# Performance work log

Measured on AMD Instinct MI355X. Metric: run time of the kernel, lower is better.

Reference implementation:

```python
import jax, jax.numpy as jnp
import numpy as np

LMAX = 3
KMAX = [128, 96, 64, 32]   # k_max_l, decreasing in l
N_ATOMS = 10000
N_EDGES = 100000
N_RADIAL = 8
CUTOFF = 5.0

def _bounds(l):
    lo = KMAX[l + 1] if l < LMAX else 0
    return lo, KMAX[l]

def _uncouple(split_list, U):
    # split_list: per l' in 0..L, [n, 2l'+1, k]; U: [3**L, (L+1)**2]
    x = jnp.concatenate(split_list, axis=1)      # [n, (L+1)**2, k]
    return jnp.einsum('dm,nmk->ndk', U, x)       # [n, 3**L, k]

def _couple(f, U, L):
    x = jnp.einsum('dm,ndk->nmk', U, f)          # [n, (L+1)**2, k]
    out, off = [], 0
    for lp in range(L + 1):
        out.append(x[:, off:off + 2 * lp + 1, :])
        off += 2 * lp + 1
    return out

def _forward(r, sh, feat, Wrad, U, Wlin, centers, neighbors):
    # radial basis with smooth cutoff, then per-l channel embedding
    n = jnp.arange(1, N_RADIAL + 1, dtype=r.dtype)
    rb = jnp.sin(n * jnp.pi * r[:, None] / CUTOFF) / (r[:, None] + 1e-6)
    fc = 0.5 * (jnp.cos(jnp.pi * jnp.clip(r / CUTOFF, 0.0, 1.0)) + 1.0)
    rb = rb * fc[:, None]                        # [E, N_RADIAL]
    radial = [rb @ Wrad[l] for l in range(LMAX + 1)]          # [E, KMAX[l]]
    vexp = [sh[l] * radial[l][:, None, :] for l in range(LMAX + 1)]  # [E, 2l+1, KMAX[l]]

    def group(ts, l):
        lo, hi = _bounds(l)
        return [ts[lp][:, :, lo:hi] for lp in range(l + 1)]

    unc_v = [_uncouple(group(vexp, l), U[l]) for l in range(LMAX + 1)]
    unc_f = [_uncouple(group(feat, l), U[l]) for l in range(LMAX + 1)]
    # neighbor gather + elementwise combine in the uncoupled (Cartesian) space
    combined = [unc_v[l] * unc_f[l][neighbors] for l in range(LMAX + 1)]
    # scatter-add pooling over centers (index_add_ equivalent)
    pooled = [jax.ops.segment_sum(c, centers, num_segments=N_ATOMS) for c in combined]
    coupled = [_couple(pooled[l], U[l], l) for l in range(LMAX + 1)]
    cat = [jnp.concatenate([coupled[lp][l] for lp in range(l, LMAX + 1)], axis=-1)
           for l in range(LMAX + 1)]             # [n_atoms, 2l+1, KMAX[l]]
    # NOTE: mp_scaling multiply in the original is dead code (result unused)
    out = [feat[l] + jnp.einsum('nmk,kq->nmq', cat[l], Wlin[l]) for l in range(LMAX + 1)]
    return tuple(out)

def setup_inputs() -> dict:
    key = jax.random.key(0)
    ks = jax.random.split(key, 40)
    inp = {'r': jax.random.uniform(ks[0], (N_EDGES,), minval=0.5, maxval=CUTOFF, dtype=jnp.float32)}
    for l in range(LMAX + 1):
        k = KMAX[l]
        inp[f'sh{l}'] = jax.random.normal(ks[1 + l], (N_EDGES, 2 * l + 1, 1), dtype=jnp.float32)
        inp[f'feat{l}'] = jax.random.normal(ks[5 + l], (N_ATOMS, 2 * l + 1, k), dtype=jnp.float32)
        inp[f'Wrad{l}'] = jax.random.normal(ks[9 + l], (N_RADIAL, k), dtype=jnp.float32) / np.sqrt(N_RADIAL).astype(np.float32)
        inp[f'U{l}'] = jax.random.normal(ks[13 + l], (3 ** l, (l + 1) ** 2), dtype=jnp.float32) / np.float32(np.sqrt((l + 1) ** 2))
        inp[f'Wlin{l}'] = jax.random.normal(ks[17 + l], (k, k), dtype=jnp.float32) / np.sqrt(k).astype(np.float32)
    inp['centers'] = jax.random.randint(ks[21], (N_EDGES,), 0, N_ATOMS, dtype=jnp.int32)
    inp['neighbors'] = jax.random.randint(ks[22], (N_EDGES,), 0, N_ATOMS, dtype=jnp.int32)
    return inp

def reference(r, sh0, sh1, sh2, sh3, feat0, feat1, feat2, feat3,
              Wrad0, Wrad1, Wrad2, Wrad3, U0, U1, U2, U3,
              Wlin0, Wlin1, Wlin2, Wlin3, centers, neighbors):
    return _forward(r, [sh0, sh1, sh2, sh3], [feat0, feat1, feat2, feat3],
                    [Wrad0, Wrad1, Wrad2, Wrad3], [U0, U1, U2, U3],
                    [Wlin0, Wlin1, Wlin2, Wlin3], centers, neighbors)
```

## Files before the change

### kernel.cpp

```cpp
#include <hip/hip_runtime.h>
#include <hip/hip_fp16.h>
#include <math.h>

#define NA 10000
#define NE 100000
#define PI_F 3.14159265358979323846f


__device__ __forceinline__ constexpr int rowC(int row) {
    return (row == 0) ? 0 : (row < 4) ? 1 : (row < 13) ? 2 : 3;
}

__device__ __forceinline__ void stage_U(const float* __restrict__ U0,
                                        const float* __restrict__ U1,
                                        const float* __restrict__ U2,
                                        const float* __restrict__ U3,
                                        float* uLds, int t, int nthr) {
    for (int i = t; i < 526; i += nthr) {
        float v;
        if (i == 0)       v = U0[0];
        else if (i < 13)  v = U1[i - 1];
        else if (i < 94)  v = U2[i - 13];
        else              v = U3[i - 94];
        uLds[i] = v;
    }
}

__global__ __launch_bounds__(256) void kCount(const int* __restrict__ centers,
                                              int* __restrict__ counts)
{
    const int e = blockIdx.x * 256 + threadIdx.x;
    if (e < NE) atomicAdd(&counts[centers[e]], 1);
}

__global__ __launch_bounds__(1024) void kScan(const int* __restrict__ counts,
                                              int* __restrict__ offsets,
                                              int* __restrict__ cursor)
{
    __shared__ int sums[1024];
    const int t = threadIdx.x;
    const int base = t * 10;
    int local[10];
    int s = 0;
#pragma unroll
    for (int j = 0; j < 10; ++j) {
        int idx = base + j;
        int v = (idx < NA) ? counts[idx] : 0;
        local[j] = s;
        s += v;
    }
    sums[t] = s;
    __syncthreads();
    for (int off = 1; off < 1024; off <<= 1) {
        int v = (t >= off) ? sums[t - off] : 0;
        __syncthreads();
        sums[t] += v;
        __syncthreads();
    }
    const int prev = (t == 0) ? 0 : sums[t - 1];
#pragma unroll
    for (int j = 0; j < 10; ++j) {
        int idx = base + j;
        if (idx <= NA) {
            int o = prev + local[j];
            offsets[idx] = o;
            if (idx < NA) cursor[idx] = o;
        }
    }
}

__global__ __launch_bounds__(256) void kPrep(
    const float* __restrict__ f0, const float* __restrict__ f1,
    const float* __restrict__ f2, const float* __restrict__ f3,
    const float* __restrict__ r,
    const float* __restrict__ sh0, const float* __restrict__ sh1,
    const float* __restrict__ sh2, const float* __restrict__ sh3,
    const float* __restrict__ U0, const float* __restrict__ U1,
    const float* __restrict__ U2, const float* __restrict__ U3,
    const int* __restrict__ centers, const int* __restrict__ neighbors,
    int* __restrict__ cursor,
    uint4* __restrict__ uncf16, float* __restrict__ rbbuf,
    uint2* __restrict__ csh, int* __restrict__ nbrs)
{
    __shared__ float uLds[526];
    const int t = threadIdx.x;
    stage_U(U0, U1, U2, U3, uLds, t, 256);
    __syncthreads();

    if (blockIdx.x < 1250) {
        const int la = t >> 5, k = t & 31;
        const int a = blockIdx.x * 8 + la;
        float arr[40];

        {
            arr[0] = uLds[0] * f0[(size_t)a * 128 + 96 + k];
        }
        {
            float x[4];
            x[0] = f0[(size_t)a * 128 + 64 + k];
#pragma unroll
            for (int m = 0; m < 3; ++m) x[1 + m] = f1[(size_t)a * 288 + m * 96 + 64 + k];
#pragma unroll
            for (int d = 0; d < 3; ++d) {
                float acc = 0.f;
#pragma unroll
                for (int m = 0; m < 4; ++m) acc += uLds[1 + d * 4 + m] * x[m];
                arr[1 + d] = acc;
            }
        }
        {
            float x[9];
            x[0] = f0[(size_t)a * 128 + 32 + k];
#pragma unroll
            for (int m = 0; m < 3; ++m) x[1 + m] = f1[(size_t)a * 288 + m * 96 + 32 + k];
#pragma unroll
            for (int m = 0; m < 5; ++m) x[4 + m] = f2[(size_t)a * 320 + m * 64 + 32 + k];
#pragma unroll
            for (int d = 0; d < 9; ++d) {
                float acc = 0.f;
#pragma unroll
                for (int m = 0; m < 9; ++m) acc += uLds[13 + d * 9 + m] * x[m];
                arr[4 + d] = acc;
            }
        }
        {
            float x[16];
            x[0] = f0[(size_t)a * 128 + k];
#pragma unroll
            for (int m = 0; m < 3; ++m) x[1 + m] = f1[(size_t)a * 288 + m * 96 + k];
#pragma unroll
            for (int m = 0; m < 5; ++m) x[4 + m] = f2[(size_t)a * 320 + m * 64 + k];
#pragma unroll
            for (int m = 0; m < 7; ++m) x[9 + m] = f3[(size_t)a * 224 + m * 32 + k];
#pragma unroll
            for (int d = 0; d < 27; ++d) {
                float acc = 0.f;
#pragma unroll
                for (int m = 0; m < 16; ++m) acc += uLds[94 + d * 16 + m] * x[m];
                arr[13 + d] = acc;
            }
        }
        uint4* op = uncf16 + (size_t)a * 160 + k;
#pragma unroll
        for (int jj = 0; jj < 5; ++jj) {
            uint4 w;
            __half2 h0 = __floats2half2_rn(arr[8 * jj + 0], arr[8 * jj + 1]);
            __half2 h1 = __floats2half2_rn(arr[8 * jj + 2], arr[8 * jj + 3]);
            __half2 h2 = __floats2half2_rn(arr[8 * jj + 4], arr[8 * jj + 5]);
            __half2 h3 = __floats2half2_rn(arr[8 * jj + 6], arr[8 * jj + 7]);
            w.x = *(unsigned int*)&h0; w.y = *(unsigned int*)&h1;
            w.z = *(unsigned int*)&h2; w.w = *(unsigned int*)&h3;
            op[jj * 32] = w;
        }
    } else {
        const int e = (blockIdx.x - 1250) * 256 + t;
        if (e >= NE) return;

        const int c_ = centers[e];
        const int pos = atomicAdd(&cursor[c_], 1);
        nbrs[pos] = neighbors[e];

        float shv[16];
        shv[0] = sh0[e];
#pragma unroll
        for (int m = 0; m < 3; ++m) shv[1 + m] = sh1[(size_t)e * 3 + m];
#pragma unroll
        for (int m = 0; m < 5; ++m) shv[4 + m] = sh2[(size_t)e * 5 + m];
#pragma unroll
        for (int m = 0; m < 7; ++m) shv[9 + m] = sh3[(size_t)e * 7 + m];

        const float rv = r[e];
        const float fc = 0.5f * (cosf(PI_F * fminf(rv * 0.2f, 1.0f)) + 1.0f);
        const float pref = fc / (rv + 1e-6f);
        const float step = rv * (PI_F * 0.2f);
        float4 ra, rb;
        ra.x = sinf(1.f * step) * pref; ra.y = sinf(2.f * step) * pref;
        ra.z = sinf(3.f * step) * pref; ra.w = sinf(4.f * step) * pref;
        rb.x = sinf(5.f * step) * pref; rb.y = sinf(6.f * step) * pref;
        rb.z = sinf(7.f * step) * pref; rb.w = sinf(8.f * step) * pref;
        *(float4*)(rbbuf + (size_t)pos * 8)     = ra;
        *(float4*)(rbbuf + (size_t)pos * 8 + 4) = rb;

        const int UO[4] = {0, 1, 13, 94};
        const int RO[4] = {0, 1, 4, 13};
        const int P3[4] = {1, 3, 9, 27};
        uint2* cso = csh + (size_t)pos * 40;
#pragma unroll
        for (int c = 0; c < 4; ++c) {
            const int M2 = (c + 1) * (c + 1);
            for (int d = 0; d < P3[c]; ++d) {
                float cv[4] = {0.f, 0.f, 0.f, 0.f};
#pragma unroll
                for (int lp = 0; lp < 4; ++lp) {
                    if (lp > c) break;
                    float s = 0.f;
#pragma unroll
                    for (int ml = 0; ml < 2 * lp + 1; ++ml)
                        s += uLds[UO[c] + d * M2 + lp * lp + ml] * shv[lp * lp + ml];
                    cv[lp] = s;
                }
                __half2 h0 = __floats2half2_rn(cv[0], cv[1]);
                __half2 h1 = __floats2half2_rn(cv[2], cv[3]);
                uint2 u;
                u.x = *(unsigned int*)&h0;
                u.y = *(unsigned int*)&h1;
                cso[RO[c] + d] = u;
            }
        }
    }
}

__global__ __launch_bounds__(256, 2) void kB2(
    const float* __restrict__ Wr0, const float* __restrict__ Wr1,
    const float* __restrict__ Wr2, const float* __restrict__ Wr3,
    const int* __restrict__ offsets, const int* __restrict__ nbrs,
    const float* __restrict__ rbbuf, const uint2* __restrict__ csh,
    const uint4* __restrict__ uncf16, float* __restrict__ pooled)
{
    __shared__ float wLds[2560];
    const int t = threadIdx.x;
    for (int i = t; i < 2560; i += 256) {
        float v;
        if (i < 1024)      v = Wr0[i];
        else if (i < 1792) v = Wr1[i - 1024];
        else if (i < 2304) v = Wr2[i - 1792];
        else               v = Wr3[i - 2304];
        wLds[i] = v;
    }
    __syncthreads();

    const int lane = t & 63;
    const int wv = t >> 6;
    const int k = lane & 31;
    const int g2 = lane >> 5;
    const int a = blockIdx.x * 4 + wv;
    const int beg = offsets[a], end = offsets[a + 1];

    float acc[40];
#pragma unroll
    for (int i = 0; i < 40; ++i) acc[i] = 0.f;

    const int KL[4] = {128, 96, 64, 32};
    const int WO[4] = {0, 1024, 1792, 2304};

    int i = beg + g2;
    int nbr = (i < end) ? nbrs[i] : 0;
    for (; i < end; i += 2) {
        const int nbr_nx = (i + 2 < end) ? nbrs[i + 2] : 0;

        const uint4* up = uncf16 + (size_t)nbr * 160 + k;
        const uint4 w0 = up[0 * 32];
        const uint4 w1 = up[1 * 32];
        const uint4 w2 = up[2 * 32];
        const uint4 w3 = up[3 * 32];
        const uint4 w4 = up[4 * 32];

        const float4 r0 = *(const float4*)(rbbuf + (size_t)i * 8);
        const float4 r1 = *(const float4*)(rbbuf + (size_t)i * 8 + 4);
        const float rb[8] = {r0.x, r0.y, r0.z, r0.w, r1.x, r1.y, r1.z, r1.w};

        float rad[4][4];
#pragma unroll
        for (int lp = 0; lp < 4; ++lp) {
#pragma unroll
            for (int c = 0; c < 4; ++c) {
                if (c < lp) continue;
                const int base = 32 * (3 - c);
                float s = 0.f;
#pragma unroll
                for (int n = 0; n < 8; ++n)
                    s += rb[n] * wLds[WO[lp] + n * KL[lp] + base + k];
                rad[lp][c] = s;
            }
        }

        const uint2* cs = csh + (size_t)i * 40;
        const uint4 ww[5] = {w0, w1, w2, w3, w4};
#pragma unroll
        for (int jj = 0; jj < 5; ++jj) {
            const unsigned int ws[4] = {ww[jj].x, ww[jj].y, ww[jj].z, ww[jj].w};
#pragma unroll
            for (int p2 = 0; p2 < 4; ++p2) {
                const int row0 = 8 * jj + 2 * p2, row1 = row0 + 1;
                const int c0 = rowC(row0), c1 = rowC(row1);
                const __half2 h = *(const __half2*)&ws[p2];
                const uint2 ua = cs[row0];
                const uint2 ub = cs[row1];
                const __half2 a01 = *(const __half2*)&ua.x;
                const __half2 a23 = *(const __half2*)&ua.y;
                const __half2 b01 = *(const __half2*)&ub.x;
                const __half2 b23 = *(const __half2*)&ub.y;
                float uv0 = __low2float(a01) * rad[0][c0];
                if (c0 >= 1) uv0 += __high2float(a01) * rad[1][c0];
                if (c0 >= 2) uv0 += __low2float(a23) * rad[2][c0];
                if (c0 >= 3) uv0 += __high2float(a23) * rad[3][c0];
                float uv1 = __low2float(b01) * rad[0][c1];
                if (c1 >= 1) uv1 += __high2float(b01) * rad[1][c1];
                if (c1 >= 2) uv1 += __low2float(b23) * rad[2][c1];
                if (c1 >= 3) uv1 += __high2float(b23) * rad[3][c1];
                acc[row0] += uv0 * __low2float(h);
                acc[row1] += uv1 * __high2float(h);
            }
        }
        nbr = nbr_nx;
    }

#pragma unroll
    for (int row = 0; row < 40; ++row) acc[row] += __shfl_xor(acc[row], 32);

    float* pp = pooled + (size_t)a * 1280 + k;
#pragma unroll
    for (int rr = 0; rr < 20; ++rr) {
        const float v   = g2 ? acc[rr + 20] : acc[rr];
        const int  row  = g2 ? (rr + 20)    : rr;
        pp[row * 32] = v;
    }
}

__global__ __launch_bounds__(256) void kC_out(
    const float* __restrict__ pooled,
    const float* __restrict__ f0, const float* __restrict__ f1,
    const float* __restrict__ f2, const float* __restrict__ f3,
    const float* __restrict__ U0, const float* __restrict__ U1,
    const float* __restrict__ U2, const float* __restrict__ U3,
    const float* __restrict__ W0, const float* __restrict__ W1,
    const float* __restrict__ W2, const float* __restrict__ W3,
    float* __restrict__ out)
{
    __shared__ float uLds[526];
    __shared__ float plds[4 * 1280];
    __shared__ float clds[120 * 33];
    const int t = threadIdx.x;
    stage_U(U0, U1, U2, U3, uLds, t, 256);
    const int a0 = blockIdx.x * 4;
    {
        const float4* src = (const float4*)(pooled + (size_t)a0 * 1280);
        float4* dst = (float4*)plds;
        for (int i = t; i < 1280; i += 256) dst[i] = src[i];
    }
    __syncthreads();

    if (t < 128) {
        const int la = t >> 5, kk = t & 31;
        clds[(la * 30 + 0) * 33 + kk] = uLds[0] * plds[la * 1280 + 0 * 32 + kk];
    }
#pragma unroll
    for (int s = t; s < 512; s += 256) {
        const int la = s >> 7, rem = s & 127;
        const int m = rem >> 5, kk = rem & 31;
        float acc = 0.f;
#pragma unroll
        for (int d = 0; d < 3; ++d)
            acc += uLds[1 + d * 4 + m] * plds[la * 1280 + (1 + d) * 32 + kk];
        clds[(la * 30 + 1 + m) * 33 + kk] = acc;
    }
    for (int s = t; s < 1152; s += 256) {
        const int la = s / 288, rem = s - la * 288;
        const int m = rem >> 5, kk = rem & 31;
        float acc = 0.f;
#pragma unroll
        for (int d = 0; d < 9; ++d)
            acc += uLds[13 + d * 9 + m] * plds[la * 1280 + (4 + d) * 32 + kk];
        clds[(la * 30 + 5 + m) * 33 + kk] = acc;
    }
    for (int s = t; s < 2048; s += 256) {
        const int la = s >> 9, rem = s & 511;
        const int m = rem >> 5, kk = rem & 31;
        float acc = 0.f;
#pragma unroll
        for (int d = 0; d < 27; ++d)
            acc += uLds[94 + d * 16 + m] * plds[la * 1280 + (13 + d) * 32 + kk];
        clds[(la * 30 + 14 + m) * 33 + kk] = acc;
    }
    __syncthreads();

    int l, m, q;
    bool active = true;
    if (t < 32)       { l = 0; m = 0;                               q = 4 * t; }
    else if (t < 104) { l = 1; int u = t - 32;  m = u / 24; q = 4 * (u % 24); }
    else if (t < 184) { l = 2; int u = t - 104; m = u / 16; q = 4 * (u % 16); }
    else if (t < 240) { l = 3; int u = t - 184; m = u / 8;  q = 4 * (u % 8);  }
    else active = false;

    if (active) {
        const int K  = (l == 0) ? 128 : (l == 1) ? 96 : (l == 2) ? 64 : 32;
        const int MK = (l == 0) ? 128 : (l == 1) ? 288 : (l == 2) ? 320 : 224;
        const size_t Ol = (l == 0) ? 0 : (l == 1) ? 1280000 : (l == 2) ? 4160000 : 7360000;
        const float* F = (l == 0) ? f0 : (l == 1) ? f1 : (l == 2) ? f2 : f3;
        const float* W = (l == 0) ? W0 : (l == 1) ? W1 : (l == 2) ? W2 : W3;
        const int CRB[4] = {0, 1, 5, 14};

        float4 acc[4];
#pragma unroll
        for (int la = 0; la < 4; ++la)
            acc[la] = *(const float4*)(F + (size_t)(a0 + la) * MK + m * K + q);

        for (int j = 0; j < 4 - l; ++j) {
            const int c = l + j;
            const int crow = CRB[c] + l * l + m;
#pragma unroll
            for (int kk = 0; kk < 32; ++kk) {
                const float4 w = *(const float4*)(W + (size_t)(32 * j + kk) * K + q);
#pragma unroll
                for (int la = 0; la < 4; ++la) {
                    const float cv = clds[(la * 30 + crow) * 33 + kk];
                    acc[la].x += cv * w.x; acc[la].y += cv * w.y;
                    acc[la].z += cv * w.z; acc[la].w += cv * w.w;
                }
            }
        }
#pragma unroll
        for (int la = 0; la < 4; ++la)
            *(float4*)(out + Ol + (size_t)(a0 + la) * MK + m * K + q) = acc[la];
    }
}

extern "C" void kernel_launch(void* const* d_in, const int* in_sizes, int n_in,
                              void* d_out, int out_size, void* d_ws, size_t ws_size,
                              hipStream_t stream)
{
    int ir, ish[4], ift[4], iwr[4], iu[4], iwl[4], ic, in_;
    if (in_sizes[2] == 300000) {
        ir = 0;
        for (int l = 0; l < 4; ++l) { ish[l] = 1 + l; ift[l] = 5 + l; iwr[l] = 9 + l; iu[l] = 13 + l; iwl[l] = 17 + l; }
        ic = 21; in_ = 22;
    } else {
        ir = 0;
        for (int l = 0; l < 4; ++l) { ish[l] = 1 + 5 * l; ift[l] = 2 + 5 * l; iwr[l] = 3 + 5 * l; iu[l] = 4 + 5 * l; iwl[l] = 5 + 5 * l; }
        ic = 21; in_ = 22;
    }
    const float* r   = (const float*)d_in[ir];
    const float* sh0 = (const float*)d_in[ish[0]];
    const float* sh1 = (const float*)d_in[ish[1]];
    const float* sh2 = (const float*)d_in[ish[2]];
    const float* sh3 = (const float*)d_in[ish[3]];
    const float* f0  = (const float*)d_in[ift[0]];
    const float* f1  = (const float*)d_in[ift[1]];
    const float* f2  = (const float*)d_in[ift[2]];
    const float* f3  = (const float*)d_in[ift[3]];
    const float* Wr0 = (const float*)d_in[iwr[0]];
    const float* Wr1 = (const float*)d_in[iwr[1]];
    const float* Wr2 = (const float*)d_in[iwr[2]];
    const float* Wr3 = (const float*)d_in[iwr[3]];
    const float* U0  = (const float*)d_in[iu[0]];
    const float* U1  = (const float*)d_in[iu[1]];
    const float* U2  = (const float*)d_in[iu[2]];
    const float* U3  = (const float*)d_in[iu[3]];
    const float* Wl0 = (const float*)d_in[iwl[0]];
    const float* Wl1 = (const float*)d_in[iwl[1]];
    const float* Wl2 = (const float*)d_in[iwl[2]];
    const float* Wl3 = (const float*)d_in[iwl[3]];
    const int* centers   = (const int*)d_in[ic];
    const int* neighbors = (const int*)d_in[in_];

    uint4* uncf16 = (uint4*)d_ws;
    float* pooled = (float*)(uncf16 + (size_t)NA * 160);
    float* rbbuf  = pooled + (size_t)NA * 1280;
    uint2* csh    = (uint2*)(rbbuf + (size_t)NE * 8);
    int*   nbrs    = (int*)(csh + (size_t)NE * 40);
    int*   counts  = nbrs + NE;
    int*   offsets = counts + NA;
    int*   cursor  = offsets + NA + 1;
    float* outp   = (float*)d_out;

    hipMemsetAsync(counts, 0, NA * sizeof(int), stream);
    kCount<<<(NE + 255) / 256, 256, 0, stream>>>(centers, counts);
    kScan<<<1, 1024, 0, stream>>>(counts, offsets, cursor);
    kPrep<<<1250 + (NE + 255) / 256, 256, 0, stream>>>(
        f0, f1, f2, f3, r, sh0, sh1, sh2, sh3, U0, U1, U2, U3,
        centers, neighbors, cursor, uncf16, rbbuf, csh, nbrs);
    kB2<<<NA / 4, 256, 0, stream>>>(Wr0, Wr1, Wr2, Wr3, offsets, nbrs,
                                    rbbuf, csh, uncf16, pooled);
    kC_out<<<NA / 4, 256, 0, stream>>>(pooled, f0, f1, f2, f3, U0, U1, U2, U3,
                                       Wl0, Wl1, Wl2, Wl3, outp);
}
```

Measured before the change: 346.9 us.

## Fuse edge-pooling and output coupling kernels through shared memory

Merges the gather/pool kernel and the couple+linear output kernel into one kernel. The pooled per-atom sums now go straight into LDS instead of a global round trip, which removes the pooled workspace buffer and one launch. The cost is a larger LDS footprint per block (about 36KB), which together with launch_bounds(256,2) may limit occupancy of the latency-bound gather phase. Load imbalance between waves of different atoms now also stalls the output phase at the block barrier.

```diff
diff --git a/kernel.cpp b/kernel.cpp
--- a/kernel.cpp
+++ b/kernel.cpp
@@ -210,14 +210,24 @@
     }
 }
 
-__global__ __launch_bounds__(256, 2) void kB2(
+__global__ __launch_bounds__(256, 2) void kBC(
     const float* __restrict__ Wr0, const float* __restrict__ Wr1,
     const float* __restrict__ Wr2, const float* __restrict__ Wr3,
     const int* __restrict__ offsets, const int* __restrict__ nbrs,
     const float* __restrict__ rbbuf, const uint2* __restrict__ csh,
-    const uint4* __restrict__ uncf16, float* __restrict__ pooled)
+    const uint4* __restrict__ uncf16,
+    const float* __restrict__ f0, const float* __restrict__ f1,
+    const float* __restrict__ f2, const float* __restrict__ f3,
+    const float* __restrict__ U0, const float* __restrict__ U1,
+    const float* __restrict__ U2, const float* __restrict__ U3,
+    const float* __restrict__ W0, const float* __restrict__ W1,
+    const float* __restrict__ W2, const float* __restrict__ W3,
+    float* __restrict__ out)
 {
     __shared__ float wLds[2560];
+    __shared__ float uLds[526];
+    __shared__ float plds[4 * 1280];
+    __shared__ float clds[120 * 33];
     const int t = threadIdx.x;
     for (int i = t; i < 2560; i += 256) {
         float v;
@@ -227,13 +237,15 @@
         else               v = Wr3[i - 2304];
         wLds[i] = v;
     }
+    stage_U(U0, U1, U2, U3, uLds, t, 256);
     __syncthreads();
 
     const int lane = t & 63;
     const int wv = t >> 6;
     const int k = lane & 31;
     const int g2 = lane >> 5;
-    const int a = blockIdx.x * 4 + wv;
+    const int a0 = blockIdx.x * 4;
+    const int a = a0 + wv;
     const int beg = offsets[a], end = offsets[a + 1];
 
     float acc[40];
@@ -308,35 +320,14 @@
 #pragma unroll
     for (int row = 0; row < 40; ++row) acc[row] += __shfl_xor(acc[row], 32);
 
-    float* pp = pooled + (size_t)a * 1280 + k;
-#pragma unroll
-    for (int rr = 0; rr < 20; ++rr) {
-        const float v   = g2 ? acc[rr + 20] : acc[rr];
-        const int  row  = g2 ? (rr + 20)    : rr;
-        pp[row * 32] = v;
-    }
-}
-
-__global__ __launch_bounds__(256) void kC_out(
-    const float* __restrict__ pooled,
-    const float* __restrict__ f0, const float* __restrict__ f1,
-    const float* __restrict__ f2, const float* __restrict__ f3,
-    const float* __restrict__ U0, const float* __restrict__ U1,
-    const float* __restrict__ U2, const float* __restrict__ U3,
-    const float* __restrict__ W0, const float* __restrict__ W1,
-    const float* __restrict__ W2, const float* __restrict__ W3,
-    float* __restrict__ out)
-{
-    __shared__ float uLds[526];
-    __shared__ float plds[4 * 1280];
-    __shared__ float clds[120 * 33];
-    const int t = threadIdx.x;
-    stage_U(U0, U1, U2, U3, uLds, t, 256);
-    const int a0 = blockIdx.x * 4;
     {
-        const float4* src = (const float4*)(pooled + (size_t)a0 * 1280);
-        float4* dst = (float4*)plds;
-        for (int i = t; i < 1280; i += 256) dst[i] = src[i];
+        float* pp = plds + wv * 1280 + k;
+#pragma unroll
+        for (int rr = 0; rr < 20; ++rr) {
+            const float v   = g2 ? acc[rr + 20] : acc[rr];
+            const int  row  = g2 ? (rr + 20)    : rr;
+            pp[row * 32] = v;
+        }
     }
     __syncthreads();
 
@@ -348,29 +339,29 @@
     for (int s = t; s < 512; s += 256) {
         const int la = s >> 7, rem = s & 127;
         const int m = rem >> 5, kk = rem & 31;
-        float acc = 0.f;
+        float accv = 0.f;
 #pragma unroll
         for (int d = 0; d < 3; ++d)
-            acc += uLds[1 + d * 4 + m] * plds[la * 1280 + (1 + d) * 32 + kk];
-        clds[(la * 30 + 1 + m) * 33 + kk] = acc;
+            accv += uLds[1 + d * 4 + m] * plds[la * 1280 + (1 + d) * 32 + kk];
+        clds[(la * 30 + 1 + m) * 33 + kk] = accv;
     }
     for (int s = t; s < 1152; s += 256) {
         const int la = s / 288, rem = s - la * 288;
         const int m = rem >> 5, kk = rem & 31;
-        float acc = 0.f;
+        float accv = 0.f;
 #pragma unroll
         for (int d = 0; d < 9; ++d)
-            acc += uLds[13 + d * 9 + m] * plds[la * 1280 + (4 + d) * 32 + kk];
-        clds[(la * 30 + 5 + m) * 33 + kk] = acc;
+            accv += uLds[13 + d * 9 + m] * plds[la * 1280 + (4 + d) * 32 + kk];
+        clds[(la * 30 + 5 + m) * 33 + kk] = accv;
     }
     for (int s = t; s < 2048; s += 256) {
         const int la = s >> 9, rem = s & 511;
         const int m = rem >> 5, kk = rem & 31;
-        float acc = 0.f;
+        float accv = 0.f;
 #pragma unroll
         for (int d = 0; d < 27; ++d)
-            acc += uLds[94 + d * 16 + m] * plds[la * 1280 + (13 + d) * 32 + kk];
-        clds[(la * 30 + 14 + m) * 33 + kk] = acc;
+            accv += uLds[94 + d * 16 + m] * plds[la * 1280 + (13 + d) * 32 + kk];
+        clds[(la * 30 + 14 + m) * 33 + kk] = accv;
     }
     __syncthreads();
 
@@ -390,10 +381,10 @@
         const float* W = (l == 0) ? W0 : (l == 1) ? W1 : (l == 2) ? W2 : W3;
         const int CRB[4] = {0, 1, 5, 14};
 
-        float4 acc[4];
+        float4 accv[4];
 #pragma unroll
         for (int la = 0; la < 4; ++la)
-            acc[la] = *(const float4*)(F + (size_t)(a0 + la) * MK + m * K + q);
+            accv[la] = *(const float4*)(F + (size_t)(a0 + la) * MK + m * K + q);
 
         for (int j = 0; j < 4 - l; ++j) {
             const int c = l + j;
@@ -404,14 +395,14 @@
 #pragma unroll
                 for (int la = 0; la < 4; ++la) {
                     const float cv = clds[(la * 30 + crow) * 33 + kk];
-                    acc[la].x += cv * w.x; acc[la].y += cv * w.y;
-                    acc[la].z += cv * w.z; acc[la].w += cv * w.w;
+                    accv[la].x += cv * w.x; accv[la].y += cv * w.y;
+                    accv[la].z += cv * w.z; accv[la].w += cv * w.w;
                 }
             }
         }
 #pragma unroll
         for (int la = 0; la < 4; ++la)
-            *(float4*)(out + Ol + (size_t)(a0 + la) * MK + m * K + q) = acc[la];
+            *(float4*)(out + Ol + (size_t)(a0 + la) * MK + m * K + q) = accv[la];
     }
 }
 
@@ -454,8 +445,7 @@
     const int* neighbors = (const int*)d_in[in_];
 
     uint4* uncf16 = (uint4*)d_ws;
-    float* pooled = (float*)(uncf16 + (size_t)NA * 160);
-    float* rbbuf  = pooled + (size_t)NA * 1280;
+    float* rbbuf  = (float*)(uncf16 + (size_t)NA * 160);
     uint2* csh    = (uint2*)(rbbuf + (size_t)NE * 8);
     int*   nbrs    = (int*)(csh + (size_t)NE * 40);
     int*   counts  = nbrs + NE;
@@ -469,8 +459,8 @@
     kPrep<<<1250 + (NE + 255) / 256, 256, 0, stream>>>(
         f0, f1, f2, f3, r, sh0, sh1, sh2, sh3, U0, U1, U2, U3,
         centers, neighbors, cursor, uncf16, rbbuf, csh, nbrs);
-    kB2<<<NA / 4, 256, 0, stream>>>(Wr0, Wr1, Wr2, Wr3, offsets, nbrs,
-                                    rbbuf, csh, uncf16, pooled);
-    kC_out<<<NA / 4, 256, 0, stream>>>(pooled, f0, f1, f2, f3, U0, U1, U2, U3,
-                                       Wl0, Wl1, Wl2, Wl3, outp);
-}
+    kBC<<<NA / 4, 256, 0, stream>>>(Wr0, Wr1, Wr2, Wr3, offsets, nbrs,
+                                    rbbuf, csh, uncf16,
+                                    f0, f1, f2, f3, U0, U1, U2, U3,
+                                    Wl0, Wl1, Wl2, Wl3, outp);
+}
```

Result: slower. 387.6 us (+11.7%).
